# Optimization experiments

Hardware: AMD Instinct MI355X
Metric: run time of the kernel (lower is better)

## Reference

```python
import jax, jax.numpy as jnp
import numpy as np

H = 2048          # hidden_size
I = 8192          # intermediate_size (shared expert)
E = 32            # num_experts
K = 4             # num_experts_per_tok
M = 1408          # moe_intermediate_size
B, S = 2, 1024


def setup_inputs() -> dict:
    key = jax.random.key(0)
    ks = jax.random.split(key, 7)
    scale = 0.02
    return {
        "hidden_states": jax.random.normal(ks[0], (B, S, H), dtype=jnp.float32),
        "gate_w": jax.random.normal(ks[1], (H, E), dtype=jnp.float32) * scale,
        "w1": jax.random.normal(ks[2], (E, H, M), dtype=jnp.float32) * scale,  # expert up-proj
        "w2": jax.random.normal(ks[3], (E, M, H), dtype=jnp.float32) * scale,  # expert down-proj
        "ws1": jax.random.normal(ks[4], (H, I), dtype=jnp.float32) * scale,    # shared up-proj
        "ws2": jax.random.normal(ks[5], (I, H), dtype=jnp.float32) * scale,    # shared down-proj
    }


def reference(hidden_states, gate_w, w1, w2, ws1, ws2):
    b, s, h = hidden_states.shape
    x = hidden_states.reshape(-1, h)                      # [T, H]

    # shared expert: Linear -> SiLU -> Linear
    shared = jax.nn.silu(x @ ws1) @ ws2                   # [T, H]

    # router: top-k logits, softmax over the k selected logits
    router_logits = x @ gate_w                            # [T, E]
    top_vals, top_idx = jax.lax.top_k(router_logits, K)   # [T, K]
    routing_weights = jax.nn.softmax(top_vals, axis=-1)   # [T, K]

    # combine weights: scatter top-k weights into dense [T, E]
    cw = (jax.nn.one_hot(top_idx, E, dtype=x.dtype)
          * routing_weights[..., None]).sum(axis=1)       # [T, E]

    # expert FFNs (dense over experts, weighted combine)
    a = jax.nn.silu(jnp.einsum('th,ehm->tem', x, w1))     # [T, E, M]
    expert_out = jnp.einsum('tem,emh,te->th', a, w2, cw)  # [T, H]

    output = (shared + expert_out).reshape(b, s, h)
    return output, router_logits.reshape(b, s, E)
```

## Files before the change

kernel.cpp:

```cpp
#include <hip/hip_runtime.h>

#define H_ 2048
#define E_ 32
#define KSEL 4
#define M_ 1408
#define I_ 8192
#define T_ 2048

typedef __bf16 bf16;
typedef bf16 bf16x8 __attribute__((ext_vector_type(8)));
typedef float f32x4 __attribute__((ext_vector_type(4)));
typedef unsigned short u16x8 __attribute__((ext_vector_type(8)));
typedef unsigned int u32x4 __attribute__((ext_vector_type(4)));

static __device__ __forceinline__ unsigned short bfb(float f) {
  return __builtin_bit_cast(unsigned short, (bf16)f);
}

static __device__ __forceinline__ void gload_lds16(const void* g, void* l) {
  __builtin_amdgcn_global_load_lds((const __attribute__((address_space(1))) void*)g,
                                   (__attribute__((address_space(3))) void*)l, 16, 0, 0);
}

static __device__ __forceinline__ float silu_f(float v) {
  return v / (1.f + __expf(-v));
}

static __device__ __forceinline__ void wave_argmax(float& v, int& vi) {
  #pragma unroll
  for (int off = 32; off >= 1; off >>= 1) {
    float ov = __shfl_xor(v, off);
    int   oi = __shfl_xor(vi, off);
    if (ov > v || (ov == v && oi < vi)) { v = ov; vi = oi; }
  }
}

__global__ __launch_bounds__(64) void prep_k(int* __restrict__ counts) {
  if (threadIdx.x < E_) counts[threadIdx.x] = 0;
}

__global__ __launch_bounds__(256) void cvt_k(const float* __restrict__ x, unsigned short* __restrict__ xb) {
  size_t i = ((size_t)blockIdx.x * 256 + threadIdx.x) * 8;
  float4 a = *(const float4*)(x + i);
  float4 b = *(const float4*)(x + i + 4);
  u16x8 o;
  o[0]=bfb(a.x); o[1]=bfb(a.y); o[2]=bfb(a.z); o[3]=bfb(a.w);
  o[4]=bfb(b.x); o[5]=bfb(b.y); o[6]=bfb(b.z); o[7]=bfb(b.w);
  *(u16x8*)(xb + i) = o;
}

__global__ __launch_bounds__(256) void combine_k(const float* __restrict__ sc,
                                                 const float* __restrict__ sc2,
                                                 float* __restrict__ out) {
  size_t i = ((size_t)blockIdx.x * 256 + threadIdx.x) * 4;
  int t = (int)(i >> 11);
  int h = (int)(i & 2047);
  const float* s = sc + (size_t)(t * 4) * H_ + h;
  float4 a = *(const float4*)(s);
  float4 b = *(const float4*)(s + H_);
  float4 c = *(const float4*)(s + 2 * H_);
  float4 d = *(const float4*)(s + 3 * H_);
  float4 o;
  o.x = a.x + b.x + c.x + d.x;
  o.y = a.y + b.y + c.y + d.y;
  o.z = a.z + b.z + c.z + d.z;
  o.w = a.w + b.w + c.w + d.w;
  #pragma unroll
  for (int kz = 0; kz < 4; ++kz) {
    float4 v = *(const float4*)(sc2 + (size_t)kz * T_ * H_ + i);
    o.x += v.x; o.y += v.y; o.z += v.z; o.w += v.w;
  }
  *(float4*)(out + i) = o;
}

__global__ __launch_bounds__(64) void router_k(const float* __restrict__ x, const float* __restrict__ gw,
                                               float* __restrict__ logits, int* __restrict__ counts,
                                               int* __restrict__ tlist, float* __restrict__ wlist) {
  int t = blockIdx.x;
  int l = threadIdx.x;
  int e = l & 31;
  int half = l >> 5;
  const float* xr = x + (size_t)t * H_ + half * (H_/2);
  const float* g  = gw + (size_t)(half * (H_/2)) * E_ + e;
  float a0=0.f, a1=0.f, a2=0.f, a3=0.f;
  for (int h = 0; h < H_/2; h += 4) {
    a0 = fmaf(xr[h],   g[(size_t)h*E_],     a0);
    a1 = fmaf(xr[h+1], g[(size_t)(h+1)*E_], a1);
    a2 = fmaf(xr[h+2], g[(size_t)(h+2)*E_], a2);
    a3 = fmaf(xr[h+3], g[(size_t)(h+3)*E_], a3);
  }
  float acc = (a0+a1)+(a2+a3);
  acc += __shfl_xor(acc, 32);
  if (l < E_) logits[(size_t)t*E_ + l] = acc;

  float cur = (l < E_) ? acc : -INFINITY;
  int myidx = (l < E_) ? e : 1000;
  float tv0,tv1,tv2,tv3; int ti0,ti1,ti2,ti3;
  { float v=cur; int vi=myidx; wave_argmax(v,vi); tv0=v; ti0=vi; if (myidx==vi) cur=-INFINITY; }
  { float v=cur; int vi=myidx; wave_argmax(v,vi); tv1=v; ti1=vi; if (myidx==vi) cur=-INFINITY; }
  { float v=cur; int vi=myidx; wave_argmax(v,vi); tv2=v; ti2=vi; if (myidx==vi) cur=-INFINITY; }
  { float v=cur; int vi=myidx; wave_argmax(v,vi); tv3=v; ti3=vi; }
  float w0 = 1.f;
  float w1 = __expf(tv1 - tv0);
  float w2 = __expf(tv2 - tv0);
  float w3 = __expf(tv3 - tv0);
  float inv = 1.f / (w0+w1+w2+w3);
  if (l < KSEL) {
    float myw = ((l==0)?w0:(l==1)?w1:(l==2)?w2:w3) * inv;
    int   myi = ((l==0)?ti0:(l==1)?ti1:(l==2)?ti2:ti3);
    int pos = atomicAdd(&counts[myi], 1);
    tlist[myi*T_ + pos] = (t << 2) | l;
    wlist[myi*T_ + pos] = myw;
  }
}

template<int MODE, int KDIM, int NDIM, int ASTR, int KSPLIT>
__global__ __launch_bounds__(256) void gemm_k(
    const bf16* __restrict__ A, const float* __restrict__ Bf,
    bf16* __restrict__ Cb, float* __restrict__ Cf,
    const int* __restrict__ tlist, const float* __restrict__ wlist,
    const int* __restrict__ counts)
{
  __shared__ __align__(16) char smem[16384];
  char* As = smem;
  char* Bs = smem + 8192;
  const int tid = threadIdx.x;

  int mt, nt, e = 0, kz = 0;
  int nrows = T_;
  const int* lst = nullptr;
  const float* Bp = Bf;
  if constexpr (MODE == 2 || MODE == 3) {
    constexpr int NT = NDIM / 128;
    constexpr int NWG = NT * E_ * 2;
    constexpr int CPX = NWG / 8;
    int id = blockIdx.x;
    int lg = (id & 7) * CPX + (id >> 3);
    int bit = lg & 1;
    int en  = lg >> 1;
    e  = en / NT;
    nt = en % NT;
    mt = (blockIdx.y == 0) ? bit : (2 + 2*((int)blockIdx.y - 1) + bit);
    nrows = counts[e];
    if (mt * 128 >= nrows) return;
    lst = tlist + e*T_;
    Bp = Bf + (size_t)e * ((size_t)KDIM * NDIM);
  } else {
    constexpr int NWG = 16 * (NDIM / 128);
    constexpr int CPX = NWG / 8;
    int id = blockIdx.x;
    int lg = (id & 7) * CPX + (id >> 3);
    mt = lg & 15;
    nt = lg >> 4;
    if constexpr (KSPLIT > 1) kz = blockIdx.z;
  }
  const int mrow0 = mt*128, ncol0 = nt*128;

  const bf16* abase[2];
  int aoffs[2];
  #pragma unroll
  for (int hh = 0; hh < 2; ++hh) {
    int lidx = hh*256 + tid;
    int row  = lidx >> 2;
    int slog = (lidx & 3) ^ (row & 3);
    aoffs[hh] = slog * 8;
    int ri = mrow0 + row;
    if constexpr (MODE == 2) {
      int tt = (ri < nrows) ? (lst[ri] >> 2) : 0;
      abase[hh] = A + (size_t)tt * ASTR;
    } else if constexpr (MODE == 3) {
      int ar = (ri < nrows) ? lst[ri] : 0;
      abase[hh] = A + (size_t)ar * ASTR;
    } else {
      abase[hh] = A + (size_t)ri * ASTR;
    }
  }

  const int bn = tid & 127;
  const int bh = tid >> 7;
  const float* bsrc0 = Bp + (size_t)(bh * 16) * NDIM + ncol0 + bn;
  char* bdst0 = Bs + (bh*2)*2048 + bn*16;

  const int l  = tid & 63;
  const int wv = tid >> 6;
  const int wr = wv >> 1, wc = wv & 1;
  const int ss = l >> 4;

  f32x4 acc[4][4] = {};

  constexpr int ITERS = KDIM / 32 / KSPLIT;
  static_assert(ITERS % 2 == 0, "K-loop is 2-unrolled");
  const int kt0 = kz * ITERS;
  const int ktend = kt0 + ITERS;

  float vA0,vA1,vA2,vA3,vA4,vA5,vA6,vA7,vA8,vA9,vA10,vA11,vA12,vA13,vA14,vA15;
  float vB0,vB1,vB2,vB3,vB4,vB5,vB6,vB7,vB8,vB9,vB10,vB11,vB12,vB13,vB14,vB15;

#define LOADB(P, KT) do {                                            \
    const float* bs_ = bsrc0 + (size_t)((KT) * 32) * NDIM;           \
    P##0 = bs_[0];            P##1 = bs_[(size_t)1*NDIM];            \
    P##2 = bs_[(size_t)2*NDIM];  P##3 = bs_[(size_t)3*NDIM];         \
    P##4 = bs_[(size_t)4*NDIM];  P##5 = bs_[(size_t)5*NDIM];         \
    P##6 = bs_[(size_t)6*NDIM];  P##7 = bs_[(size_t)7*NDIM];         \
    P##8 = bs_[(size_t)8*NDIM];  P##9 = bs_[(size_t)9*NDIM];         \
    P##10 = bs_[(size_t)10*NDIM]; P##11 = bs_[(size_t)11*NDIM];      \
    P##12 = bs_[(size_t)12*NDIM]; P##13 = bs_[(size_t)13*NDIM];      \
    P##14 = bs_[(size_t)14*NDIM]; P##15 = bs_[(size_t)15*NDIM];      \
  } while (0)

#define WRITEB(P) do {                                               \
    u32x4 lo_, hi_;                                                  \
    lo_[0] = (unsigned)bfb(P##0)  | ((unsigned)bfb(P##1)  << 16);    \
    lo_[1] = (unsigned)bfb(P##2)  | ((unsigned)bfb(P##3)  << 16);    \
    lo_[2] = (unsigned)bfb(P##4)  | ((unsigned)bfb(P##5)  << 16);    \
    lo_[3] = (unsigned)bfb(P##6)  | ((unsigned)bfb(P##7)  << 16);    \
    hi_[0] = (unsigned)bfb(P##8)  | ((unsigned)bfb(P##9)  << 16);    \
    hi_[1] = (unsigned)bfb(P##10) | ((unsigned)bfb(P##11) << 16);    \
    hi_[2] = (unsigned)bfb(P##12) | ((unsigned)bfb(P##13) << 16);    \
    hi_[3] = (unsigned)bfb(P##14) | ((unsigned)bfb(P##15) << 16);    \
    *(u32x4*)(bdst0)        = lo_;                                   \
    *(u32x4*)(bdst0 + 2048) = hi_;                                   \
  } while (0)

#define MFMA_PHASE(KT) do {                                          \
    bf16x8 af[4], bfr[4];                                            \
    _Pragma("unroll")                                                \
    for (int mf = 0; mf < 4; ++mf) {                                 \
      int r = wr*64 + mf*16 + (l & 15);                              \
      af[mf] = *(const bf16x8*)(As + r*64 + ((ss ^ (r & 3)) << 4));  \
    }                                                                \
    _Pragma("unroll")                                                \
    for (int nf = 0; nf < 4; ++nf) {                                 \
      int c = wc*64 + nf*16 + (l & 15);                              \
      bfr[nf] = *(const bf16x8*)(Bs + ss*2048 + c*16);               \
    }                                                                \
    _Pragma("unroll")                                                \
    for (int mf = 0; mf < 4; ++mf)                                   \
      _Pragma("unroll")                                              \
      for (int nf = 0; nf < 4; ++nf)                                 \
        acc[mf][nf] = __builtin_amdgcn_mfma_f32_16x16x32_bf16(af[mf], bfr[nf], acc[mf][nf], 0, 0, 0); \
  } while (0)

#define ADMA(KT) do {                                                \
    _Pragma("unroll")                                                \
    for (int hh = 0; hh < 2; ++hh)                                   \
      gload_lds16(abase[hh] + (KT)*32 + aoffs[hh], As + (hh*256 + tid)*16); \
  } while (0)

  LOADB(vA, kt0);
  for (int kt = kt0; kt < ktend; kt += 2) {
    __syncthreads();
    ADMA(kt);
    WRITEB(vA);
    __syncthreads();
    LOADB(vB, kt + 1);
    MFMA_PHASE(kt);

    __syncthreads();
    ADMA(kt + 1);
    WRITEB(vB);
    __syncthreads();
    if (kt + 2 < ktend) LOADB(vA, kt + 2);
    MFMA_PHASE(kt + 1);
  }

#undef LOADB
#undef WRITEB
#undef MFMA_PHASE
#undef ADMA

  #pragma unroll
  for (int mf = 0; mf < 4; ++mf) {
    #pragma unroll
    for (int j = 0; j < 4; ++j) {
      const int rloc = wr*64 + mf*16 + (l >> 4)*4 + j;
      const int grow = mrow0 + rloc;
      if constexpr (MODE == 0) {
        #pragma unroll
        for (int nf = 0; nf < 4; ++nf) {
          int col = ncol0 + wc*64 + nf*16 + (l & 15);
          Cb[(size_t)grow * NDIM + col] = (bf16)silu_f(acc[mf][nf][j]);
        }
      } else if constexpr (MODE == 1) {
        float* dst = Cf + (size_t)kz * T_ * H_;
        #pragma unroll
        for (int nf = 0; nf < 4; ++nf) {
          int col = ncol0 + wc*64 + nf*16 + (l & 15);
          dst[(size_t)grow * NDIM + col] = acc[mf][nf][j];
        }
      } else if constexpr (MODE == 2) {
        if (grow < nrows) {
          int entry = lst[grow];
          float wg = wlist[e*T_ + grow];
          #pragma unroll
          for (int nf = 0; nf < 4; ++nf) {
            int col = ncol0 + wc*64 + nf*16 + (l & 15);
            Cb[(size_t)entry * NDIM + col] = (bf16)(silu_f(acc[mf][nf][j]) * wg);
          }
        }
      } else {
        if (grow < nrows) {
          int entry = lst[grow];
          #pragma unroll
          for (int nf = 0; nf < 4; ++nf) {
            int col = ncol0 + wc*64 + nf*16 + (l & 15);
            Cf[(size_t)entry * H_ + col] = acc[mf][nf][j];
          }
        }
      }
    }
  }
}

extern "C" void kernel_launch(void* const* d_in, const int* in_sizes, int n_in,
                              void* d_out, int out_size, void* d_ws, size_t ws_size,
                              hipStream_t stream) {
  const float* x   = (const float*)d_in[0];
  const float* gw  = (const float*)d_in[1];
  const float* w1  = (const float*)d_in[2];
  const float* w2  = (const float*)d_in[3];
  const float* ws1 = (const float*)d_in[4];
  const float* ws2 = (const float*)d_in[5];
  float* out    = (float*)d_out;
  float* logits = out + (size_t)T_ * H_;

  char* ws = (char*)d_ws;
  const size_t off_xb   = 0;
  const size_t off_y1   = off_xb  + (size_t)T_ * H_ * 2;
  const size_t off_act  = off_y1  + (size_t)T_ * I_ * 2;
  const size_t off_cnt  = off_act + (size_t)T_ * 4 * M_ * 2;
  const size_t off_tl   = off_cnt + 256;
  const size_t off_wl   = off_tl  + (size_t)E_ * T_ * 4;
  const size_t off_sc   = off_wl  + (size_t)E_ * T_ * 4;
  const size_t off_sc2  = off_sc  + (size_t)T_ * 4 * H_ * 4;

  const bf16* xb = (const bf16*)(ws + off_xb);
  bf16* y1  = (bf16*)(ws + off_y1);
  bf16* act = (bf16*)(ws + off_act);
  int*  counts = (int*)(ws + off_cnt);
  int*  tlist  = (int*)(ws + off_tl);
  float* wlist = (float*)(ws + off_wl);
  float* scratch  = (float*)(ws + off_sc);
  float* scratch2 = (float*)(ws + off_sc2);

  prep_k<<<1, 64, 0, stream>>>(counts);
  router_k<<<T_, 64, 0, stream>>>(x, gw, logits, counts, tlist, wlist);
  cvt_k<<<2048, 256, 0, stream>>>(x, (unsigned short*)(ws + off_xb));

  gemm_k<0, 2048, 8192, 2048, 1><<<dim3(1024), 256, 0, stream>>>(
      xb, ws1, y1, nullptr, nullptr, nullptr, nullptr);
  gemm_k<1, 8192, 2048, 8192, 4><<<dim3(256, 1, 4), 256, 0, stream>>>(
      y1, ws2, nullptr, scratch2, nullptr, nullptr, nullptr);
  gemm_k<2, 2048, 1408, 2048, 1><<<dim3(11*E_*2, 8), 256, 0, stream>>>(
      xb, w1, act, nullptr, tlist, wlist, counts);
  gemm_k<3, 1408, 2048, 1408, 1><<<dim3(16*E_*2, 8), 256, 0, stream>>>(
      act, w2, nullptr, scratch, tlist, nullptr, counts);
  combine_k<<<4096, 256, 0, stream>>>(scratch, scratch2, out);
}
```

Measured before the change: 830.4 us.

## Double-buffer LDS tiles to halve barriers in GEMM K-loop

Doubles shared memory to two A/B tile buffers, so the next tile's async A load and B register-to-LDS write go into one buffer while MFMAs read the other. The K-loop now has one barrier per tile instead of two, which cuts sync stalls and overlaps DMA with compute. In exchange LDS use per block goes from 16KB to 32KB, which may lower occupancy. Register pressure rises because the two B prefetch register sets are live at the same time.

```diff
diff --git a/kernel.cpp b/kernel.cpp
--- a/kernel.cpp
+++ b/kernel.cpp
@@ -121,9 +121,7 @@
     const int* __restrict__ tlist, const float* __restrict__ wlist,
     const int* __restrict__ counts)
 {
-  __shared__ __align__(16) char smem[16384];
-  char* As = smem;
-  char* Bs = smem + 8192;
+  __shared__ __align__(16) char smem[32768];
   const int tid = threadIdx.x;
 
   int mt, nt, e = 0, kz = 0;
@@ -179,7 +177,7 @@
   const int bn = tid & 127;
   const int bh = tid >> 7;
   const float* bsrc0 = Bp + (size_t)(bh * 16) * NDIM + ncol0 + bn;
-  char* bdst0 = Bs + (bh*2)*2048 + bn*16;
+  const int bdoff = (bh*2)*2048 + bn*16;
 
   const int l  = tid & 63;
   const int wv = tid >> 6;
@@ -208,7 +206,7 @@
     P##14 = bs_[(size_t)14*NDIM]; P##15 = bs_[(size_t)15*NDIM];      \
   } while (0)
 
-#define WRITEB(P) do {                                               \
+#define WRITEB(P, BUF) do {                                          \
     u32x4 lo_, hi_;                                                  \
     lo_[0] = (unsigned)bfb(P##0)  | ((unsigned)bfb(P##1)  << 16);    \
     lo_[1] = (unsigned)bfb(P##2)  | ((unsigned)bfb(P##3)  << 16);    \
@@ -218,21 +216,24 @@
     hi_[1] = (unsigned)bfb(P##10) | ((unsigned)bfb(P##11) << 16);    \
     hi_[2] = (unsigned)bfb(P##12) | ((unsigned)bfb(P##13) << 16);    \
     hi_[3] = (unsigned)bfb(P##14) | ((unsigned)bfb(P##15) << 16);    \
-    *(u32x4*)(bdst0)        = lo_;                                   \
-    *(u32x4*)(bdst0 + 2048) = hi_;                                   \
+    char* bd_ = smem + (BUF)*16384 + 8192 + bdoff;                   \
+    *(u32x4*)(bd_)        = lo_;                                     \
+    *(u32x4*)(bd_ + 2048) = hi_;                                     \
   } while (0)
 
-#define MFMA_PHASE(KT) do {                                          \
+#define MFMA_PHASE(BUF) do {                                         \
+    const char* As_ = smem + (BUF)*16384;                            \
+    const char* Bs_ = smem + (BUF)*16384 + 8192;                     \
     bf16x8 af[4], bfr[4];                                            \
     _Pragma("unroll")                                                \
     for (int mf = 0; mf < 4; ++mf) {                                 \
       int r = wr*64 + mf*16 + (l & 15);                              \
-      af[mf] = *(const bf16x8*)(As + r*64 + ((ss ^ (r & 3)) << 4));  \
+      af[mf] = *(const bf16x8*)(As_ + r*64 + ((ss ^ (r & 3)) << 4)); \
     }                                                                \
     _Pragma("unroll")                                                \
     for (int nf = 0; nf < 4; ++nf) {                                 \
       int c = wc*64 + nf*16 + (l & 15);                              \
-      bfr[nf] = *(const bf16x8*)(Bs + ss*2048 + c*16);               \
+      bfr[nf] = *(const bf16x8*)(Bs_ + ss*2048 + c*16);              \
     }                                                                \
     _Pragma("unroll")                                                \
     for (int mf = 0; mf < 4; ++mf)                                   \
@@ -241,27 +242,33 @@
         acc[mf][nf] = __builtin_amdgcn_mfma_f32_16x16x32_bf16(af[mf], bfr[nf], acc[mf][nf], 0, 0, 0); \
   } while (0)
 
-#define ADMA(KT) do {                                                \
+#define ADMA(KT, BUF) do {                                           \
     _Pragma("unroll")                                                \
     for (int hh = 0; hh < 2; ++hh)                                   \
-      gload_lds16(abase[hh] + (KT)*32 + aoffs[hh], As + (hh*256 + tid)*16); \
+      gload_lds16(abase[hh] + (KT)*32 + aoffs[hh],                   \
+                  smem + (BUF)*16384 + (hh*256 + tid)*16);           \
   } while (0)
 
   LOADB(vA, kt0);
+  ADMA(kt0, 0);
+  WRITEB(vA, 0);
+  LOADB(vB, kt0 + 1);
+  __syncthreads();
+
   for (int kt = kt0; kt < ktend; kt += 2) {
+    const bool more2 = (kt + 2 < ktend);
+    ADMA(kt + 1, 1);
+    WRITEB(vB, 1);
+    if (more2) LOADB(vA, kt + 2);
+    MFMA_PHASE(0);
     __syncthreads();
-    ADMA(kt);
-    WRITEB(vA);
+    if (more2) {
+      ADMA(kt + 2, 0);
+      WRITEB(vA, 0);
+    }
+    if (kt + 3 < ktend) LOADB(vB, kt + 3);
+    MFMA_PHASE(1);
     __syncthreads();
-    LOADB(vB, kt + 1);
-    MFMA_PHASE(kt);
-
-    __syncthreads();
-    ADMA(kt + 1);
-    WRITEB(vB);
-    __syncthreads();
-    if (kt + 2 < ktend) LOADB(vA, kt + 2);
-    MFMA_PHASE(kt + 1);
   }
 
 #undef LOADB
```

Result: no change. 831.4 us (+0.1%).
